# Kernel tuning notes

Measured on AMD Instinct MI355X. Metric: run time of the kernel, lower is better.

Reference implementation:

```python
import jax, jax.numpy as jnp
import numpy as np

# Structure constants (equal-sized graphs; first SPG nodes of each graph are sentence nodes)
B = 64          # graphs in batch
NPG = 1024      # nodes per graph
SPG = 64        # sentence nodes per graph
N = B * NPG     # 65536 total nodes
E = 524288      # total edges (within-graph)
C = 256         # in_channels
H = 512         # TopKPooling hardcoded hidden
KS = 3          # num_output_sentences
KO = int(np.ceil(0.5 * (NPG - SPG)))  # ratio=0.5 -> 480 'other' nodes kept per graph
SLOPE = 0.01    # LeakyReLU default negative slope


def gcn_conv(x, row, col, w, W, b, n):
    """PyG GCNConv with edge_weight: add self-loops (weight 1), symmetric norm, aggregate at col."""
    loop = jnp.arange(n, dtype=row.dtype)
    row2 = jnp.concatenate([row, loop])
    col2 = jnp.concatenate([col, loop])
    w2 = jnp.concatenate([w, jnp.ones((n,), w.dtype)])
    deg = jax.ops.segment_sum(w2, col2, num_segments=n)
    dinv = jnp.where(deg > 0, jax.lax.rsqrt(jnp.where(deg > 0, deg, 1.0)), 0.0)
    norm = dinv[row2] * w2 * dinv[col2]          # [E+N]
    h = x @ W                                     # [N, out]
    out = jax.ops.segment_sum(norm[:, None] * h[row2], col2, num_segments=n)
    return out + b


def setup_inputs() -> dict:
    key = jax.random.key(0)
    ks = jax.random.split(key, 6)
    x = jax.random.normal(ks[0], (N, C), jnp.float32)
    # within-graph random edges
    gid = jnp.arange(E, dtype=jnp.int32) // (E // B)
    src = jax.random.randint(ks[1], (E,), 0, NPG, dtype=jnp.int32) + gid * NPG
    dst = jax.random.randint(ks[2], (E,), 0, NPG, dtype=jnp.int32) + gid * NPG
    edge_index = jnp.stack([src, dst], axis=0)
    edge_attr = jax.random.uniform(ks[3], (E, 1), jnp.float32, 0.1, 1.0)
    batch = jnp.repeat(jnp.arange(B, dtype=jnp.int32), NPG)
    W1 = jax.random.normal(ks[4], (C, H), jnp.float32) * (1.0 / np.sqrt(C))
    b1 = jnp.zeros((H,), jnp.float32)
    W2 = jax.random.normal(ks[5], (H, 1), jnp.float32) * (1.0 / np.sqrt(H))
    b2 = jnp.zeros((1,), jnp.float32)
    return {"x": x, "edge_index": edge_index, "edge_attr": edge_attr, "batch": batch,
            "W1": W1, "b1": b1, "W2": W2, "b2": b2}


def reference(x, edge_index, edge_attr, batch, W1, b1, W2, b2):
    row, col = edge_index[0], edge_index[1]
    w = edge_attr[:, 0]                           # edge_weight = edge_attr.squeeze()
    # 2-layer GCN scorer
    h = gcn_conv(x, row, col, w, W1, b1, N)
    h = jnp.where(h > 0, h, SLOPE * h)            # LeakyReLU
    score = gcn_conv(h, row, col, w, W2, b2, N)[:, 0]
    score = jnp.nan_to_num(score)
    sg = score.reshape(B, NPG)                    # dense per-graph scores (graphs equal-sized)
    # per-graph top-k: 3 sentence nodes, ceil(0.5*other) other nodes
    _, si = jax.lax.top_k(sg[:, :SPG], KS)        # [B, KS] local idx among sentence nodes
    sent_perm = (si + jnp.arange(B)[:, None] * NPG).reshape(-1)
    _, oi = jax.lax.top_k(sg[:, SPG:], KO)        # [B, KO] local idx among other nodes
    other_perm = (oi + SPG + jnp.arange(B)[:, None] * NPG).reshape(-1)
    perm = jnp.concatenate([sent_perm, other_perm])  # [B*(KS+KO)]
    # gather + scale (multiplier = 1)
    score_perm = score[perm]
    x_out = x[perm] * score_perm[:, None]
    batch_out = batch[perm]
    # filter_adj (padded: dropped edges marked -1 / zeroed; 'keep' mask returned)
    mask = jnp.full((N,), -1, dtype=perm.dtype).at[perm].set(jnp.arange(perm.shape[0], dtype=perm.dtype))
    nr, nc = mask[row], mask[col]
    keep = (nr >= 0) & (nc >= 0)
    ei_new = jnp.where(keep, jnp.stack([nr, nc], axis=0), -1)
    ea_new = jnp.where(keep[:, None], edge_attr, 0.0)
    sentence_scores = sg[:, :SPG].reshape(-1)
    sentence_batch = jnp.repeat(jnp.arange(B, dtype=batch.dtype), SPG)
    return (x_out, ei_new, ea_new, batch_out, perm, score_perm, sentence_scores, sentence_batch, keep)
```

## Files before the change

### kernel.cpp

```cpp
#include <hip/hip_runtime.h>

#define NN   65536
#define NE   524288
#define EPG  8192

#define O1 7913472
#define O2 8962048
#define O3 9486336
#define O4 9517248
#define O5 9548160
#define O6 9579072
#define O7 9583168
#define O8 9587264

#define CSR_OFF    8388608
#define DINV_OFF   9437184
#define Z_OFF      9502720
#define W1HI_OFF   9568256
#define RSTART_OFF 9633792
#define CURSOR_OFF 9699344
#define W1LO_OFF   9764880
#define HIST_OFF   9830416
#define SCORE_OFF  65536
#define YLO_OFF    4194304

typedef __attribute__((ext_vector_type(8))) short bfrag;
typedef __attribute__((ext_vector_type(4))) float f32x4;
typedef __attribute__((ext_vector_type(8))) unsigned short us8;
typedef __attribute__((ext_vector_type(2))) unsigned long long u64x2;

__device__ __forceinline__ unsigned monof(float f) {
  unsigned u = __float_as_uint(f);
  return (u & 0x80000000u) ? ~u : (u | 0x80000000u);
}

__device__ __forceinline__ unsigned short bf16rne(float f) {
  unsigned u = __float_as_uint(f);
  return (unsigned short)((u + 0x7FFFu + ((u >> 16) & 1u)) >> 16);
}

__global__ void k_zero(unsigned long long* __restrict__ hist, float* __restrict__ z) {
  int n = blockIdx.x * 256 + threadIdx.x;
  if (n < NN) { hist[n] = 0ull; z[n] = 0.0f; }
}

__global__ void k_hist(const int* __restrict__ ei, const float* __restrict__ w,
                       unsigned long long* __restrict__ hist) {
  int e = blockIdx.x * 256 + threadIdx.x;
  if (e < NE) {
    int c = ei[NE + e];
    unsigned long long add = (1ull << 40) |
        (unsigned long long)(unsigned)__float2uint_rn(w[e] * 1048576.0f);
    atomicAdd(&hist[c], add);
  }
}

__global__ __launch_bounds__(256) void k_prefix(const unsigned long long* __restrict__ hist,
    unsigned* __restrict__ rstart, unsigned* __restrict__ cursor, float* __restrict__ dinv) {
  __shared__ unsigned tmp[2][256];
  int g = blockIdx.x, t = threadIdx.x;
  int base = g << 10;
  unsigned c[4], sum = 0;
  unsigned long long hv[4];
#pragma unroll
  for (int u = 0; u < 4; ++u) {
    hv[u] = hist[base + t * 4 + u];
    c[u] = (unsigned)(hv[u] >> 40);
    sum += c[u];
  }
  tmp[0][t] = sum;
  __syncthreads();
  int pin = 0;
  for (int off = 1; off < 256; off <<= 1) {
    int pout = pin ^ 1;
    unsigned v = tmp[pin][t];
    if (t >= off) v += tmp[pin][t - off];
    tmp[pout][t] = v;
    __syncthreads();
    pin = pout;
  }
  unsigned run = (t == 0) ? 0u : tmp[pin][t - 1];
#pragma unroll
  for (int u = 0; u < 4; ++u) {
    unsigned pos = (unsigned)(g << 13) + run;
    rstart[base + t * 4 + u] = pos;
    cursor[base + t * 4 + u] = pos;
    run += c[u];
  }
#pragma unroll
  for (int u = 0; u < 4; ++u) {
    int n = base + t * 4 + u;
    float wsum = 1.0f + (float)(hv[u] & ((1ull << 40) - 1)) * 9.5367431640625e-07f;
    dinv[n] = rsqrtf(wsum);
  }
  if (g == 0 && t == 0) rstart[NN] = NE;
}

__global__ __launch_bounds__(256) void k_w1t(const float* __restrict__ W1,
    unsigned short* __restrict__ hi, unsigned short* __restrict__ lo) {
  __shared__ unsigned short sh[64][72], sl[64][72];
  int bk = blockIdx.x & 3, bc = blockIdx.x >> 2;
  int k0 = bk * 64, c0 = bc * 64;
  int t = threadIdx.x;
#pragma unroll
  for (int s = 0; s < 16; ++s) {
    int i = t + s * 256;
    int k = i >> 6, c = i & 63;
    float v = W1[(k0 + k) * 512 + c0 + c];
    unsigned short h = bf16rne(v);
    float hf = __uint_as_float((unsigned)h << 16);
    sh[c][k] = h;
    sl[c][k] = bf16rne(v - hf);
  }
  __syncthreads();
#pragma unroll
  for (int s = 0; s < 16; ++s) {
    int i = t + s * 256;
    int c = i >> 6, k = i & 63;
    hi[(c0 + c) * 256 + k0 + k] = sh[c][k];
    lo[(c0 + c) * 256 + k0 + k] = sl[c][k];
  }
}

__global__ void k_scatter(const int* __restrict__ ei, const float* __restrict__ w,
                          const float* __restrict__ dinv, unsigned* __restrict__ cursor,
                          unsigned long long* __restrict__ csr) {
  int e = blockIdx.x * 256 + threadIdx.x;
  if (e < NE) {
    int r = ei[e], c = ei[NE + e];
    float cf = w[e] * dinv[r] * dinv[c];
    unsigned pos = atomicAdd(&cursor[c], 1u);
    csr[pos] = ((unsigned long long)__float_as_uint(cf) << 32) |
               ((unsigned)(c & 1023) << 16) | (unsigned)(r & 1023);
  }
}

__global__ __launch_bounds__(1024, 1) void k_aggx(const float* __restrict__ x,
    const unsigned long long* __restrict__ csr, const unsigned* __restrict__ rstart,
    const float* __restrict__ dinv, unsigned short* __restrict__ yhi,
    unsigned short* __restrict__ ylo, int gbase) {
  __shared__ float xs[1024 * 17];
  __shared__ unsigned long long es[8192];
  __shared__ unsigned rp[1025];
  __shared__ float dv2[1024];
  int bid = blockIdx.x;
  int g  = bid & 31;
  int cc = bid >> 5;
  int gg = gbase + g;
  int c0 = cc * 16;
  int t = threadIdx.x;
  int nbase = gg << 10;
  unsigned ebase = (unsigned)gg << 13;
  {
    int i = t;
    if (i < 1024) {
      rp[i] = rstart[nbase + i] - ebase;
      float dv = dinv[nbase + i];
      dv2[i] = dv * dv;
    }
  }
  if (t == 0) rp[1024] = 8192u;
  {
    const u64x2* src = (const u64x2*)(csr + ebase);
    u64x2* dst = (u64x2*)es;
#pragma unroll
    for (int i = 0; i < 4; ++i)
      dst[t + i * 1024] = src[t + i * 1024];
  }
#pragma unroll
  for (int s = 0; s < 4; ++s) {
    int i = t + s * 1024;
    int row = i >> 2, q = (i & 3) * 4;
    float4 v = *(const float4*)&x[(nbase + row) * 256 + c0 + q];
    float* d = &xs[row * 17 + q];
    d[0] = v.x; d[1] = v.y; d[2] = v.z; d[3] = v.w;
  }
  __syncthreads();
  int j = t & 15, grp = t >> 4;
  int dbase = grp * 16;
  for (int dd = 0; dd < 8; ++dd) {
    int d0 = dbase + dd, d1 = d0 + 8;
    unsigned p0 = rp[d0], q0 = rp[d0 + 1];
    unsigned p1 = rp[d1], q1 = rp[d1 + 1];
    int L0 = (int)(q0 - p0), L1 = (int)(q1 - p1);
    int L = L0 > L1 ? L0 : L1;
    int M0 = L0 > 0 ? L0 - 1 : 0;
    int M1 = L1 > 0 ? L1 - 1 : 0;
    float a0 = dv2[d0] * xs[d0 * 17 + j];
    float a1 = dv2[d1] * xs[d1 * 17 + j];
    for (int k = 0; k < L; k += 4) {
      unsigned long long cv0[4], cv1[4];
#pragma unroll
      for (int u = 0; u < 4; ++u) {
        int kk = k + u;
        int i0 = kk < M0 ? kk : M0;
        int i1 = kk < M1 ? kk : M1;
        cv0[u] = es[p0 + i0];
        cv1[u] = es[p1 + i1];
      }
#pragma unroll
      for (int u = 0; u < 4; ++u) {
        int kk = k + u;
        float f0 = kk < L0 ? __uint_as_float((unsigned)(cv0[u] >> 32)) : 0.0f;
        float f1 = kk < L1 ? __uint_as_float((unsigned)(cv1[u] >> 32)) : 0.0f;
        a0 += f0 * xs[(unsigned)(cv0[u] & 1023) * 17 + j];
        a1 += f1 * xs[(unsigned)(cv1[u] & 1023) * 17 + j];
      }
    }
    int i0 = ((g << 10) + d0) * 256 + c0 + j;
    int i1 = ((g << 10) + d1) * 256 + c0 + j;
    unsigned short h0 = bf16rne(a0), h1 = bf16rne(a1);
    yhi[i0] = h0;
    ylo[i0] = bf16rne(a0 - __uint_as_float((unsigned)h0 << 16));
    yhi[i1] = h1;
    ylo[i1] = bf16rne(a1 - __uint_as_float((unsigned)h1 << 16));
  }
}

__global__ __launch_bounds__(256, 2) void k_gemm(
    const unsigned short* __restrict__ yhi, const unsigned short* __restrict__ ylo,
    const unsigned short* __restrict__ w1hi, const unsigned short* __restrict__ w1lo,
    const float* __restrict__ b1, const float* __restrict__ W2,
    float* __restrict__ z, int node_base) {
  __shared__ unsigned short Ah_s[128 * 40], Al_s[128 * 40];
  __shared__ unsigned short Bh_s[128 * 40], Bl_s[128 * 40];
  int bx = blockIdx.x & 3, by = blockIdx.x >> 2;
  int r0 = by * 128, c0 = bx * 128;
  int t = threadIdx.x;
  int lane = t & 63, wid = t >> 6;
  int wr = wid >> 1, wc = wid & 1;
  int lr = lane & 15, hg = lane >> 4;
  f32x4 acc[4][4];
#pragma unroll
  for (int m = 0; m < 4; ++m)
#pragma unroll
    for (int n = 0; n < 4; ++n)
      acc[m][n] = (f32x4){0.0f, 0.0f, 0.0f, 0.0f};
  int rr = t >> 2, kq = (t & 3) * 8;
  for (int kt = 0; kt < 256; kt += 32) {
    us8 va0 = *(const us8*)&yhi[(r0 + rr) * 256 + kt + kq];
    us8 va1 = *(const us8*)&yhi[(r0 + rr + 64) * 256 + kt + kq];
    us8 vb0 = *(const us8*)&ylo[(r0 + rr) * 256 + kt + kq];
    us8 vb1 = *(const us8*)&ylo[(r0 + rr + 64) * 256 + kt + kq];
    us8 vc0 = *(const us8*)&w1hi[(c0 + rr) * 256 + kt + kq];
    us8 vc1 = *(const us8*)&w1hi[(c0 + rr + 64) * 256 + kt + kq];
    us8 vd0 = *(const us8*)&w1lo[(c0 + rr) * 256 + kt + kq];
    us8 vd1 = *(const us8*)&w1lo[(c0 + rr + 64) * 256 + kt + kq];
    __syncthreads();
    *(us8*)&Ah_s[rr * 40 + kq] = va0;  *(us8*)&Ah_s[(rr + 64) * 40 + kq] = va1;
    *(us8*)&Al_s[rr * 40 + kq] = vb0;  *(us8*)&Al_s[(rr + 64) * 40 + kq] = vb1;
    *(us8*)&Bh_s[rr * 40 + kq] = vc0;  *(us8*)&Bh_s[(rr + 64) * 40 + kq] = vc1;
    *(us8*)&Bl_s[rr * 40 + kq] = vd0;  *(us8*)&Bl_s[(rr + 64) * 40 + kq] = vd1;
    __syncthreads();
    bfrag Ah[4], Al[4], Bh[4], Bl[4];
#pragma unroll
    for (int m = 0; m < 4; ++m) {
      int ra = (wr * 64 + m * 16 + lr) * 40 + hg * 8;
      Ah[m] = *(const bfrag*)&Ah_s[ra];
      Al[m] = *(const bfrag*)&Al_s[ra];
      int rb = (wc * 64 + m * 16 + lr) * 40 + hg * 8;
      Bh[m] = *(const bfrag*)&Bh_s[rb];
      Bl[m] = *(const bfrag*)&Bl_s[rb];
    }
#pragma unroll
    for (int m = 0; m < 4; ++m)
#pragma unroll
      for (int n = 0; n < 4; ++n) {
        acc[m][n] = __builtin_amdgcn_mfma_f32_16x16x32_bf16(Ah[m], Bh[n], acc[m][n], 0, 0, 0);
        acc[m][n] = __builtin_amdgcn_mfma_f32_16x16x32_bf16(Ah[m], Bl[n], acc[m][n], 0, 0, 0);
        acc[m][n] = __builtin_amdgcn_mfma_f32_16x16x32_bf16(Al[m], Bh[n], acc[m][n], 0, 0, 0);
      }
  }
  float p[4][4];
#pragma unroll
  for (int m = 0; m < 4; ++m)
#pragma unroll
    for (int i = 0; i < 4; ++i) p[m][i] = 0.0f;
#pragma unroll
  for (int n = 0; n < 4; ++n) {
    int col = c0 + wc * 64 + n * 16 + lr;
    float b1v = b1[col], w2v = W2[col];
#pragma unroll
    for (int m = 0; m < 4; ++m)
#pragma unroll
      for (int i = 0; i < 4; ++i) {
        float v = acc[m][n][i] + b1v;
        v = v > 0.0f ? v : 0.01f * v;
        p[m][i] += v * w2v;
      }
  }
#pragma unroll
  for (int off = 8; off > 0; off >>= 1)
#pragma unroll
    for (int m = 0; m < 4; ++m)
#pragma unroll
      for (int i = 0; i < 4; ++i)
        p[m][i] += __shfl_xor(p[m][i], off, 16);
  if (lr == 0) {
    int rbase = node_base + r0 + wr * 64 + hg * 4;
#pragma unroll
    for (int m = 0; m < 4; ++m)
#pragma unroll
      for (int i = 0; i < 4; ++i)
        unsafeAtomicAdd(&z[rbase + m * 16 + i], p[m][i]);
  }
}

__global__ void k_score(const unsigned long long* __restrict__ csr,
                        const unsigned* __restrict__ rstart,
                        const float* __restrict__ dinv, const float* __restrict__ z,
                        const float* __restrict__ b2, float* __restrict__ score,
                        int* __restrict__ mask) {
  int n = blockIdx.x * 256 + threadIdx.x;
  if (n >= NN) return;
  mask[n] = -1;
  int nb = n & ~1023;
  float dv = dinv[n];
  float a = b2[0] + dv * dv * z[n];
  unsigned s = rstart[n], epos = rstart[n + 1];
  for (unsigned e = s; e < epos; ++e) {
    unsigned long long p = csr[e];
    a += __uint_as_float((unsigned)(p >> 32)) * z[nb + (unsigned)(p & 1023)];
  }
  score[n] = a;
}

__device__ void bitonic(unsigned long long* keys, int n, int t, int nt) {
  for (int k = 2; k <= n; k <<= 1)
    for (int jj = k >> 1; jj > 0; jj >>= 1) {
      __syncthreads();
      for (int i = t; i < n; i += nt) {
        int ixj = i ^ jj;
        if (ixj > i) {
          unsigned long long a = keys[i], c = keys[ixj];
          bool up = ((i & k) == 0);
          if ((a > c) == up) { keys[i] = c; keys[ixj] = a; }
        }
      }
    }
  __syncthreads();
}

__global__ __launch_bounds__(256) void k_topk(const float* __restrict__ score,
                                              int* __restrict__ mask,
                                              float* __restrict__ out) {
  __shared__ unsigned long long keys[1024];
  int b = blockIdx.x, t = threadIdx.x;
  int base = b << 10;
  if (t < 64) {
    float v = score[base + t];
    keys[t] = ((unsigned long long)(~monof(v)) << 32) | (unsigned)t;
    out[O6 + b * 64 + t] = v;
    out[O7 + b * 64 + t] = (float)b;
  }
  __syncthreads();
  bitonic(keys, 64, t, 256);
  if (t < 3) {
    int idx = (int)(keys[t] & 0xFFFFFFFFull);
    int node = base + idx;
    int pos = b * 3 + t;
    mask[node] = pos;
    out[O4 + pos] = (float)node;
    out[O5 + pos] = score[node];
    out[O3 + pos] = (float)b;
  }
  __syncthreads();
  for (int i = t; i < 1024; i += 256) {
    if (i < 960) {
      float v = score[base + 64 + i];
      keys[i] = ((unsigned long long)(~monof(v)) << 32) | (unsigned)i;
    } else {
      keys[i] = 0xFFFFFFFFFFFFFFFFull;
    }
  }
  __syncthreads();
  bitonic(keys, 1024, t, 256);
  for (int r = t; r < 480; r += 256) {
    int idx = (int)(keys[r] & 0xFFFFFFFFull);
    int node = base + 64 + idx;
    int pos = 192 + b * 480 + r;
    mask[node] = pos;
    out[O4 + pos] = (float)node;
    out[O5 + pos] = score[node];
    out[O3 + pos] = (float)b;
  }
}

__global__ void k_edges(const int* __restrict__ ei, const float* __restrict__ w,
                        const int* __restrict__ mask, float* __restrict__ out) {
  int e = blockIdx.x * 256 + threadIdx.x;
  if (e >= NE) return;
  int nr = mask[ei[e]];
  int nc = mask[ei[NE + e]];
  bool keep = (nr >= 0) && (nc >= 0);
  out[O1 + e]      = keep ? (float)nr : -1.0f;
  out[O1 + NE + e] = keep ? (float)nc : -1.0f;
  out[O2 + e]      = keep ? w[e] : 0.0f;
  out[O8 + e]      = keep ? 1.0f : 0.0f;
}

__global__ void k_xout(const float* __restrict__ x, const float* __restrict__ permF,
                       const float* __restrict__ scoreP, float* __restrict__ out) {
  int i = blockIdx.x;
  int node = (int)permF[i];
  float s = scoreP[i];
  const float4* xr = (const float4*)&x[node * 256];
  float4* o = (float4*)&out[i * 256];
  float4 v = xr[threadIdx.x];
  o[threadIdx.x] = make_float4(v.x * s, v.y * s, v.z * s, v.w * s);
}

extern "C" void kernel_launch(void* const* d_in, const int* in_sizes, int n_in,
                              void* d_out, int out_size, void* d_ws, size_t ws_size,
                              hipStream_t stream) {
  (void)in_sizes; (void)n_in; (void)out_size; (void)d_ws; (void)ws_size;
  const float* x  = (const float*)d_in[0];
  const int*   ei = (const int*)d_in[1];
  const float* w  = (const float*)d_in[2];
  const float* W1 = (const float*)d_in[4];
  const float* b1 = (const float*)d_in[5];
  const float* W2 = (const float*)d_in[6];
  const float* b2 = (const float*)d_in[7];
  float* out    = (float*)d_out;
  unsigned short* yhi = (unsigned short*)out;
  unsigned short* ylo = (unsigned short*)(out + YLO_OFF);
  unsigned long long* csr = (unsigned long long*)(out + CSR_OFF);
  float* dinv   = out + DINV_OFF;
  float* z      = out + Z_OFF;
  unsigned* rstart = (unsigned*)(out + RSTART_OFF);
  unsigned* cursor = (unsigned*)(out + CURSOR_OFF);
  unsigned long long* hist64 = (unsigned long long*)(out + HIST_OFF);
  unsigned short* w1hi = (unsigned short*)(out + W1HI_OFF);
  unsigned short* w1lo = (unsigned short*)(out + W1LO_OFF);
  float* score  = out + SCORE_OFF;
  int*   mask   = (int*)d_out;

  k_zero<<<256, 256, 0, stream>>>(hist64, z);
  k_hist<<<2048, 256, 0, stream>>>(ei, w, hist64);
  k_prefix<<<64, 256, 0, stream>>>(hist64, rstart, cursor, dinv);
  k_w1t<<<32, 256, 0, stream>>>(W1, w1hi, w1lo);
  k_scatter<<<2048, 256, 0, stream>>>(ei, w, dinv, cursor, csr);
  for (int ch = 0; ch < 2; ++ch) {
    k_aggx<<<512, 1024, 0, stream>>>(x, csr, rstart, dinv, yhi, ylo, ch * 32);
    k_gemm<<<1024, 256, 0, stream>>>(yhi, ylo, w1hi, w1lo, b1, W2, z, ch * 32768);
  }
  k_score<<<256, 256, 0, stream>>>(csr, rstart, dinv, z, b2, score, mask);
  k_topk<<<64, 256, 0, stream>>>(score, mask, out);
  k_edges<<<2048, 256, 0, stream>>>(ei, w, mask, out);
  k_xout<<<30912, 64, 0, stream>>>(x, out + O4, out + O5, out);
}
```

Before: 259.5 us.

## Vectorize edge aggregation with float2 channel pairs and pre-scaled CSR offsets

Changes the per-edge CSR packing so the low bits hold the source row already multiplied by an 18-float stride, which removes the index multiply in the inner loop. The shared x tile is padded to 18 floats per row so it can be read as float2. Each thread now handles two channels of a single destination node instead of one channel of two nodes. Out-of-range edge slots point at a zero sentinel entry rather than being masked per lane. Output writes are packed into 32-bit stores. The trade-off is possible shared-memory bank conflicts from the new stride and greater load imbalance between the two half-groups.

```diff
diff --git a/kernel.cpp b/kernel.cpp
--- a/kernel.cpp
+++ b/kernel.cpp
@@ -130,8 +130,9 @@
     int r = ei[e], c = ei[NE + e];
     float cf = w[e] * dinv[r] * dinv[c];
     unsigned pos = atomicAdd(&cursor[c], 1u);
+    unsigned sl = (unsigned)(r & 1023);
     csr[pos] = ((unsigned long long)__float_as_uint(cf) << 32) |
-               ((unsigned)(c & 1023) << 16) | (unsigned)(r & 1023);
+               (sl << 15) | (sl * 18u);
   }
 }
 
@@ -139,8 +140,8 @@
     const unsigned long long* __restrict__ csr, const unsigned* __restrict__ rstart,
     const float* __restrict__ dinv, unsigned short* __restrict__ yhi,
     unsigned short* __restrict__ ylo, int gbase) {
-  __shared__ float xs[1024 * 17];
-  __shared__ unsigned long long es[8192];
+  __shared__ float xs[1024 * 18];
+  __shared__ unsigned long long es[8193];
   __shared__ unsigned rp[1025];
   __shared__ float dv2[1024];
   int bid = blockIdx.x;
@@ -152,14 +153,11 @@
   int nbase = gg << 10;
   unsigned ebase = (unsigned)gg << 13;
   {
-    int i = t;
-    if (i < 1024) {
-      rp[i] = rstart[nbase + i] - ebase;
-      float dv = dinv[nbase + i];
-      dv2[i] = dv * dv;
-    }
-  }
-  if (t == 0) rp[1024] = 8192u;
+    rp[t] = rstart[nbase + t] - ebase;
+    float dv = dinv[nbase + t];
+    dv2[t] = dv * dv;
+  }
+  if (t == 0) { rp[1024] = 8192u; es[8192] = 0ull; }
   {
     const u64x2* src = (const u64x2*)(csr + ebase);
     u64x2* dst = (u64x2*)es;
@@ -172,48 +170,49 @@
     int i = t + s * 1024;
     int row = i >> 2, q = (i & 3) * 4;
     float4 v = *(const float4*)&x[(nbase + row) * 256 + c0 + q];
-    float* d = &xs[row * 17 + q];
-    d[0] = v.x; d[1] = v.y; d[2] = v.z; d[3] = v.w;
-  }
-  __syncthreads();
-  int j = t & 15, grp = t >> 4;
+    float* d = &xs[row * 18 + q];
+    *(float2*)&d[0] = make_float2(v.x, v.y);
+    *(float2*)&d[2] = make_float2(v.z, v.w);
+  }
+  __syncthreads();
+  int jj = t & 7;
+  int h  = (t >> 3) & 1;
+  int grp = t >> 4;
   int dbase = grp * 16;
+  int j2 = 2 * jj;
   for (int dd = 0; dd < 8; ++dd) {
-    int d0 = dbase + dd, d1 = d0 + 8;
-    unsigned p0 = rp[d0], q0 = rp[d0 + 1];
-    unsigned p1 = rp[d1], q1 = rp[d1 + 1];
-    int L0 = (int)(q0 - p0), L1 = (int)(q1 - p1);
+    int d0 = dbase + dd;
+    unsigned pA = rp[d0], qA = rp[d0 + 1];
+    unsigned pB = rp[d0 + 8], qB = rp[d0 + 9];
+    int L0 = (int)(qA - pA), L1 = (int)(qB - pB);
     int L = L0 > L1 ? L0 : L1;
-    int M0 = L0 > 0 ? L0 - 1 : 0;
-    int M1 = L1 > 0 ? L1 - 1 : 0;
-    float a0 = dv2[d0] * xs[d0 * 17 + j];
-    float a1 = dv2[d1] * xs[d1 * 17 + j];
+    int d = d0 + 8 * h;
+    unsigned p = h ? pB : pA;
+    unsigned q = h ? qB : qA;
+    float2 xv = *(const float2*)&xs[d * 18 + j2];
+    float dv = dv2[d];
+    float ax = dv * xv.x, ay = dv * xv.y;
     for (int k = 0; k < L; k += 4) {
-      unsigned long long cv0[4], cv1[4];
+      unsigned long long cv[4];
 #pragma unroll
       for (int u = 0; u < 4; ++u) {
-        int kk = k + u;
-        int i0 = kk < M0 ? kk : M0;
-        int i1 = kk < M1 ? kk : M1;
-        cv0[u] = es[p0 + i0];
-        cv1[u] = es[p1 + i1];
+        unsigned a = p + (unsigned)(k + u);
+        cv[u] = es[a < q ? a : 8192u];
       }
 #pragma unroll
       for (int u = 0; u < 4; ++u) {
-        int kk = k + u;
-        float f0 = kk < L0 ? __uint_as_float((unsigned)(cv0[u] >> 32)) : 0.0f;
-        float f1 = kk < L1 ? __uint_as_float((unsigned)(cv1[u] >> 32)) : 0.0f;
-        a0 += f0 * xs[(unsigned)(cv0[u] & 1023) * 17 + j];
-        a1 += f1 * xs[(unsigned)(cv1[u] & 1023) * 17 + j];
+        float cf = __uint_as_float((unsigned)(cv[u] >> 32));
+        const float2 xr = *(const float2*)&xs[((unsigned)cv[u] & 0x7FFFu) + j2];
+        ax += cf * xr.x;
+        ay += cf * xr.y;
       }
     }
-    int i0 = ((g << 10) + d0) * 256 + c0 + j;
-    int i1 = ((g << 10) + d1) * 256 + c0 + j;
-    unsigned short h0 = bf16rne(a0), h1 = bf16rne(a1);
-    yhi[i0] = h0;
-    ylo[i0] = bf16rne(a0 - __uint_as_float((unsigned)h0 << 16));
-    yhi[i1] = h1;
-    ylo[i1] = bf16rne(a1 - __uint_as_float((unsigned)h1 << 16));
+    int idx = ((g << 10) + d) * 256 + c0 + j2;
+    unsigned short hx = bf16rne(ax), hy = bf16rne(ay);
+    float lx = ax - __uint_as_float((unsigned)hx << 16);
+    float ly = ay - __uint_as_float((unsigned)hy << 16);
+    *(unsigned*)&yhi[idx] = (unsigned)hx | ((unsigned)hy << 16);
+    *(unsigned*)&ylo[idx] = (unsigned)bf16rne(lx) | ((unsigned)bf16rne(ly) << 16);
   }
 }
 
@@ -320,7 +319,7 @@
   unsigned s = rstart[n], epos = rstart[n + 1];
   for (unsigned e = s; e < epos; ++e) {
     unsigned long long p = csr[e];
-    a += __uint_as_float((unsigned)(p >> 32)) * z[nb + (unsigned)(p & 1023)];
+    a += __uint_as_float((unsigned)(p >> 32)) * z[nb + (((unsigned)p >> 15) & 1023u)];
   }
   score[n] = a;
 }
```

After: 251.2 us. 1.03x faster.
